# Kernel optimization log

Measured on AMD Instinct MI355X. Metric: run time of the kernel, lower is better.

Reference implementation:

```python
import jax, jax.numpy as jnp
import numpy as np

KERNEL = 301  # sliding max window length (odd -> same-size output)
TOPK = 2


def setup_inputs() -> dict:
    key = jax.random.key(0)
    xcorr = jax.random.normal(key, (32, 3, 64, 8192), dtype=jnp.float32)
    return {"xcorr": xcorr, "nlag": 4096}


def reference(xcorr, nlag):
    # xcorr: [nb, nc, nx, nt]
    x = jnp.abs(xcorr)  # vabs=True
    pad = KERNEL // 2
    # sliding-window max over time axis (== F.max_pool2d((1,K), stride 1, pad K//2))
    smax = jax.lax.reduce_window(
        x,
        -jnp.inf,
        jax.lax.max,
        window_dimensions=(1, 1, 1, KERNEL),
        window_strides=(1, 1, 1, 1),
        padding=[(0, 0), (0, 0), (0, 0), (pad, pad)],
    )
    # keep only local maxima, zero elsewhere (x * (smax == x).float())
    scores = jnp.where(smax == x, x, jnp.zeros((), x.dtype))
    topk_score, topk_idx = jax.lax.top_k(scores, TOPK)  # [nb, nc, nx, TOPK]
    return topk_score, topk_idx
```

## Files before the change

### kernel.cpp

```cpp
#include <hip/hip_runtime.h>
#include <stdint.h>


#define NT 8192
#define RADIUS 150
#define NSEG 256

__global__ __launch_bounds__(256, 8) void seg_pass(
    const float* __restrict__ x, float2* __restrict__ ws)
{
    const int row = blockIdx.x;
    const int tid = threadIdx.x;
    const float4* g4 = (const float4*)(x + (size_t)row * NT);
    float2* wrow = ws + (size_t)row * NSEG;

    float4 vv[8];
#pragma unroll
    for (int it = 0; it < 8; ++it) vv[it] = g4[it * 256 + tid];

    const int sh = (tid & 7) * 4;
#pragma unroll
    for (int it = 0; it < 8; ++it) {
        const float4 v = vv[it];
        const float ax = fabsf(v.x), ay = fabsf(v.y);
        const float az = fabsf(v.z), aw = fabsf(v.w);
        const float cm4 = fmaxf(fmaxf(ax, ay), fmaxf(az, aw));
        float cm = fmaxf(cm4, __shfl_xor(cm4, 1));
        cm = fmaxf(cm, __shfl_xor(cm, 2));
        cm = fmaxf(cm, __shfl_xor(cm, 4));
        unsigned msk = ((ax == cm ? 1u : 0u) |
                        (ay == cm ? 2u : 0u) |
                        (az == cm ? 4u : 0u) |
                        (aw == cm ? 8u : 0u)) << sh;
        msk |= __shfl_xor((int)msk, 1);
        msk |= __shfl_xor((int)msk, 2);
        msk |= __shfl_xor((int)msk, 4);
        if ((tid & 7) == 0) {
            const int seg = (it * 256 + tid) >> 3;
            wrow[seg] = make_float2(cm, __uint_as_float(msk));
        }
    }
}

__global__ __launch_bounds__(256) void peaks_pass(
    const float* __restrict__ x, const float2* __restrict__ ws,
    float* __restrict__ out, int nrows)
{
    const int row = blockIdx.x;
    const int s = threadIdx.x;

    __shared__ float mm[8 + NSEG + 16];
    __shared__ unsigned long long wred[8];
    float* const mmp = mm + 8;

    const float2 w = ws[(size_t)row * NSEG + s];
    const float sval = w.x;
    unsigned msk = __float_as_uint(w.y);

    if (s < 8) mm[s] = 0.0f;
    if (s < 16) mm[8 + NSEG + s] = 0.0f;
    mmp[s] = sval;
    __syncthreads();

    const float4* g4 = (const float4*)(x + (size_t)row * NT);
    unsigned long long k1 = 0ull, k2 = 0ull;

    while (msk) {
        const int b = __builtin_ctz(msk); msk &= (msk - 1u);
        const int t = (s << 5) + b;
        const float val = sval;
        const int l = max(t - RADIUS, 0);
        const int r = min(t + RADIUS, NT - 1);
        const int il = l >> 5, ir = r >> 5;
        const int len = ir - il - 1;
        const float* mp = &mmp[il + 1];
        float iv[9];
#pragma unroll
        for (int j = 0; j < 9; ++j) iv[j] = mp[j];
        float im = 0.0f;
#pragma unroll
        for (int j = 0; j < 9; ++j) im = fmaxf(im, (j < len) ? iv[j] : 0.0f);
        if (im > val) continue;
        float em = 0.0f;
        {
            const int hb0 = l >> 2;
            const int hbN = il * 8 + 8;
#pragma unroll
            for (int j = 0; j < 8; ++j) {
                const int bb = hb0 + j;
                const float4 q = g4[bb];
                float bm;
                if (j == 0) {
                    bm = (4 * bb + 0 >= l) ? fabsf(q.x) : 0.0f;
                    bm = fmaxf(bm, (4 * bb + 1 >= l) ? fabsf(q.y) : 0.0f);
                    bm = fmaxf(bm, (4 * bb + 2 >= l) ? fabsf(q.z) : 0.0f);
                    bm = fmaxf(bm, fabsf(q.w));
                } else {
                    bm = fmaxf(fmaxf(fabsf(q.x), fabsf(q.y)),
                               fmaxf(fabsf(q.z), fabsf(q.w)));
                }
                em = fmaxf(em, (bb < hbN) ? bm : 0.0f);
            }
        }
        {
            const int tb0 = ir * 8;
#pragma unroll
            for (int j = 0; j < 8; ++j) {
                const int bb = tb0 + j;
                const float4 q = g4[bb];
                float bm;
                bm = (4 * bb + 0 <= r) ? fabsf(q.x) : 0.0f;
                bm = fmaxf(bm, (4 * bb + 1 <= r) ? fabsf(q.y) : 0.0f);
                bm = fmaxf(bm, (4 * bb + 2 <= r) ? fabsf(q.z) : 0.0f);
                bm = fmaxf(bm, (4 * bb + 3 <= r) ? fabsf(q.w) : 0.0f);
                em = fmaxf(em, bm);
            }
        }
        if (em > val) continue;
        const unsigned long long key =
            ((unsigned long long)__float_as_uint(val) << 32) |
            (unsigned)(NT - 1 - t);
        if (key > k1) { k2 = k1; k1 = key; }
        else if (key > k2) { k2 = key; }
    }

#pragma unroll
    for (int off = 32; off >= 1; off >>= 1) {
        unsigned long long o1 = __shfl_down(k1, off);
        unsigned long long o2 = __shfl_down(k2, off);
        unsigned long long hi = (k1 > o1) ? k1 : o1;
        unsigned long long lo = (k1 > o1) ? o1 : k1;
        unsigned long long s2 = (k2 > o2) ? k2 : o2;
        k1 = hi;
        k2 = (lo > s2) ? lo : s2;
    }
    const int wave = s >> 6;
    if ((s & 63) == 0) { wred[wave * 2] = k1; wred[wave * 2 + 1] = k2; }
    __syncthreads();

    if (s == 0) {
        unsigned long long a1 = wred[0], a2 = wred[1];
        for (int wv = 1; wv < 4; ++wv) {
            unsigned long long o1 = wred[wv * 2], o2 = wred[wv * 2 + 1];
            unsigned long long hi = (a1 > o1) ? a1 : o1;
            unsigned long long lo = (a1 > o1) ? o1 : a1;
            unsigned long long s2 = (a2 > o2) ? a2 : o2;
            a1 = hi;
            a2 = (lo > s2) ? lo : s2;
        }
        float s1v, s2v; int i1, i2;
        if (a1 == 0ull) { s1v = 0.0f; i1 = 0; }
        else {
            s1v = __uint_as_float((unsigned)(a1 >> 32));
            i1 = (NT - 1) - (int)(a1 & 0xffffffffull);
        }
        if (a2 == 0ull) {
            s2v = 0.0f;
            i2 = (i1 == 0) ? 1 : 0;
        } else {
            s2v = __uint_as_float((unsigned)(a2 >> 32));
            i2 = (NT - 1) - (int)(a2 & 0xffffffffull);
        }
        out[row * 2 + 0] = s1v;
        out[row * 2 + 1] = s2v;
        float* oi = out + (size_t)nrows * 2;
        oi[row * 2 + 0] = (float)i1;
        oi[row * 2 + 1] = (float)i2;
    }
}

extern "C" void kernel_launch(void* const* d_in, const int* in_sizes, int n_in,
                              void* d_out, int out_size, void* d_ws, size_t ws_size,
                              hipStream_t stream) {
    const float* x = (const float*)d_in[0];
    float* out = (float*)d_out;
    const int nrows = in_sizes[0] / NT;
    float2* ws = (float2*)d_ws;
    seg_pass<<<nrows, 256, 0, stream>>>(x, ws);
    peaks_pass<<<nrows, 256, 0, stream>>>(x, ws, out, nrows);
}
```

Baseline: 300.8 us.

## Fuse segment-max pass into peak detection kernel and prefilter by neighbor segments

Merges the two kernels into one. Each thread now loads its own 32-element segment directly, computes the segment max in registers and publishes it to shared memory, which removes the workspace write/read round trip and one launch. It also adds an early rejection: if any segment within three positions either side exceeds this segment's max, all candidates in the segment are skipped before the per-candidate checks. Per-thread loads are no longer interleaved across threads (each thread reads 8 consecutive float4), which may reduce coalescing, and register use rises from holding the loaded values.

```diff
diff --git a/kernel.cpp b/kernel.cpp
--- a/kernel.cpp
+++ b/kernel.cpp
@@ -6,45 +6,8 @@
 #define RADIUS 150
 #define NSEG 256
 
-__global__ __launch_bounds__(256, 8) void seg_pass(
-    const float* __restrict__ x, float2* __restrict__ ws)
-{
-    const int row = blockIdx.x;
-    const int tid = threadIdx.x;
-    const float4* g4 = (const float4*)(x + (size_t)row * NT);
-    float2* wrow = ws + (size_t)row * NSEG;
-
-    float4 vv[8];
-#pragma unroll
-    for (int it = 0; it < 8; ++it) vv[it] = g4[it * 256 + tid];
-
-    const int sh = (tid & 7) * 4;
-#pragma unroll
-    for (int it = 0; it < 8; ++it) {
-        const float4 v = vv[it];
-        const float ax = fabsf(v.x), ay = fabsf(v.y);
-        const float az = fabsf(v.z), aw = fabsf(v.w);
-        const float cm4 = fmaxf(fmaxf(ax, ay), fmaxf(az, aw));
-        float cm = fmaxf(cm4, __shfl_xor(cm4, 1));
-        cm = fmaxf(cm, __shfl_xor(cm, 2));
-        cm = fmaxf(cm, __shfl_xor(cm, 4));
-        unsigned msk = ((ax == cm ? 1u : 0u) |
-                        (ay == cm ? 2u : 0u) |
-                        (az == cm ? 4u : 0u) |
-                        (aw == cm ? 8u : 0u)) << sh;
-        msk |= __shfl_xor((int)msk, 1);
-        msk |= __shfl_xor((int)msk, 2);
-        msk |= __shfl_xor((int)msk, 4);
-        if ((tid & 7) == 0) {
-            const int seg = (it * 256 + tid) >> 3;
-            wrow[seg] = make_float2(cm, __uint_as_float(msk));
-        }
-    }
-}
-
-__global__ __launch_bounds__(256) void peaks_pass(
-    const float* __restrict__ x, const float2* __restrict__ ws,
-    float* __restrict__ out, int nrows)
+__global__ __launch_bounds__(256) void detect_peaks_kernel(
+    const float* __restrict__ x, float* __restrict__ out, int nrows)
 {
     const int row = blockIdx.x;
     const int s = threadIdx.x;
@@ -53,75 +16,100 @@
     __shared__ unsigned long long wred[8];
     float* const mmp = mm + 8;
 
-    const float2 w = ws[(size_t)row * NSEG + s];
-    const float sval = w.x;
-    unsigned msk = __float_as_uint(w.y);
+    const float4* g4 = (const float4*)(x + (size_t)row * NT);
 
     if (s < 8) mm[s] = 0.0f;
     if (s < 16) mm[8 + NSEG + s] = 0.0f;
+
+    float4 vv[8];
+#pragma unroll
+    for (int j = 0; j < 8; ++j) vv[j] = g4[s * 8 + j];
+
+    float sval = 0.0f;
+#pragma unroll
+    for (int j = 0; j < 8; ++j) {
+        float4 v = vv[j];
+        v.x = fabsf(v.x); v.y = fabsf(v.y);
+        v.z = fabsf(v.z); v.w = fabsf(v.w);
+        vv[j] = v;
+        sval = fmaxf(sval, fmaxf(fmaxf(v.x, v.y), fmaxf(v.z, v.w)));
+    }
     mmp[s] = sval;
     __syncthreads();
 
-    const float4* g4 = (const float4*)(x + (size_t)row * NT);
+    float nbr[9];
+#pragma unroll
+    for (int j = 0; j < 9; ++j) nbr[j] = mmp[s - 4 + j];
+    float nb7 = 0.0f;
+#pragma unroll
+    for (int j = 1; j <= 7; ++j) nb7 = fmaxf(nb7, nbr[j]);
+
     unsigned long long k1 = 0ull, k2 = 0ull;
 
-    while (msk) {
-        const int b = __builtin_ctz(msk); msk &= (msk - 1u);
-        const int t = (s << 5) + b;
-        const float val = sval;
-        const int l = max(t - RADIUS, 0);
-        const int r = min(t + RADIUS, NT - 1);
-        const int il = l >> 5, ir = r >> 5;
-        const int len = ir - il - 1;
-        const float* mp = &mmp[il + 1];
-        float iv[9];
+    if (!(nb7 > sval)) {
+        unsigned eqm = 0u;
 #pragma unroll
-        for (int j = 0; j < 9; ++j) iv[j] = mp[j];
-        float im = 0.0f;
+        for (int j = 0; j < 8; ++j) {
+            eqm |= (vv[j].x == sval ? 1u : 0u) << (4 * j + 0);
+            eqm |= (vv[j].y == sval ? 1u : 0u) << (4 * j + 1);
+            eqm |= (vv[j].z == sval ? 1u : 0u) << (4 * j + 2);
+            eqm |= (vv[j].w == sval ? 1u : 0u) << (4 * j + 3);
+        }
+        while (eqm) {
+            const int b = __builtin_ctz(eqm); eqm &= (eqm - 1u);
+            const int t = (s << 5) + b;
+            const int l = max(t - RADIUS, 0);
+            const int r = min(t + RADIUS, NT - 1);
+            const int il = l >> 5, ir = r >> 5;
+            float im = 0.0f;
 #pragma unroll
-        for (int j = 0; j < 9; ++j) im = fmaxf(im, (j < len) ? iv[j] : 0.0f);
-        if (im > val) continue;
-        float em = 0.0f;
-        {
-            const int hb0 = l >> 2;
-            const int hbN = il * 8 + 8;
+            for (int j = 0; j < 9; ++j) {
+                const int seg = s - 4 + j;
+                im = fmaxf(im, (seg >= il + 1 && seg <= ir - 1) ? nbr[j] : 0.0f);
+            }
+            if (im > sval) continue;
+            float em = 0.0f;
+            {
+                const int hb0 = l >> 2;
+                const int hbN = il * 8 + 8;
 #pragma unroll
-            for (int j = 0; j < 8; ++j) {
-                const int bb = hb0 + j;
-                const float4 q = g4[bb];
-                float bm;
-                if (j == 0) {
-                    bm = (4 * bb + 0 >= l) ? fabsf(q.x) : 0.0f;
-                    bm = fmaxf(bm, (4 * bb + 1 >= l) ? fabsf(q.y) : 0.0f);
-                    bm = fmaxf(bm, (4 * bb + 2 >= l) ? fabsf(q.z) : 0.0f);
-                    bm = fmaxf(bm, fabsf(q.w));
-                } else {
-                    bm = fmaxf(fmaxf(fabsf(q.x), fabsf(q.y)),
-                               fmaxf(fabsf(q.z), fabsf(q.w)));
+                for (int j = 0; j < 8; ++j) {
+                    const int bb = hb0 + j;
+                    const float4 q = g4[bb];
+                    float bm;
+                    if (j == 0) {
+                        bm = (4 * bb + 0 >= l) ? fabsf(q.x) : 0.0f;
+                        bm = fmaxf(bm, (4 * bb + 1 >= l) ? fabsf(q.y) : 0.0f);
+                        bm = fmaxf(bm, (4 * bb + 2 >= l) ? fabsf(q.z) : 0.0f);
+                        bm = fmaxf(bm, fabsf(q.w));
+                    } else {
+                        bm = fmaxf(fmaxf(fabsf(q.x), fabsf(q.y)),
+                                   fmaxf(fabsf(q.z), fabsf(q.w)));
+                    }
+                    em = fmaxf(em, (bb < hbN) ? bm : 0.0f);
                 }
-                em = fmaxf(em, (bb < hbN) ? bm : 0.0f);
             }
+            {
+                const int tb0 = ir * 8;
+#pragma unroll
+                for (int j = 0; j < 8; ++j) {
+                    const int bb = tb0 + j;
+                    const float4 q = g4[bb];
+                    float bm;
+                    bm = (4 * bb + 0 <= r) ? fabsf(q.x) : 0.0f;
+                    bm = fmaxf(bm, (4 * bb + 1 <= r) ? fabsf(q.y) : 0.0f);
+                    bm = fmaxf(bm, (4 * bb + 2 <= r) ? fabsf(q.z) : 0.0f);
+                    bm = fmaxf(bm, (4 * bb + 3 <= r) ? fabsf(q.w) : 0.0f);
+                    em = fmaxf(em, bm);
+                }
+            }
+            if (em > sval) continue;
+            const unsigned long long key =
+                ((unsigned long long)__float_as_uint(sval) << 32) |
+                (unsigned)(NT - 1 - t);
+            if (key > k1) { k2 = k1; k1 = key; }
+            else if (key > k2) { k2 = key; }
         }
-        {
-            const int tb0 = ir * 8;
-#pragma unroll
-            for (int j = 0; j < 8; ++j) {
-                const int bb = tb0 + j;
-                const float4 q = g4[bb];
-                float bm;
-                bm = (4 * bb + 0 <= r) ? fabsf(q.x) : 0.0f;
-                bm = fmaxf(bm, (4 * bb + 1 <= r) ? fabsf(q.y) : 0.0f);
-                bm = fmaxf(bm, (4 * bb + 2 <= r) ? fabsf(q.z) : 0.0f);
-                bm = fmaxf(bm, (4 * bb + 3 <= r) ? fabsf(q.w) : 0.0f);
-                em = fmaxf(em, bm);
-            }
-        }
-        if (em > val) continue;
-        const unsigned long long key =
-            ((unsigned long long)__float_as_uint(val) << 32) |
-            (unsigned)(NT - 1 - t);
-        if (key > k1) { k2 = k1; k1 = key; }
-        else if (key > k2) { k2 = key; }
     }
 
 #pragma unroll
@@ -175,7 +163,5 @@
     const float* x = (const float*)d_in[0];
     float* out = (float*)d_out;
     const int nrows = in_sizes[0] / NT;
-    float2* ws = (float2*)d_ws;
-    seg_pass<<<nrows, 256, 0, stream>>>(x, ws);
-    peaks_pass<<<nrows, 256, 0, stream>>>(x, ws, out, nrows);
+    detect_peaks_kernel<<<nrows, 256, 0, stream>>>(x, out, nrows);
 }
```

Result: faster. 273.8 us (-9.0%).
